# Kernel optimization log

Measured on AMD Instinct MI355X. Metric: run time of the kernel, lower is better.

Reference implementation:

```python
import jax, jax.numpy as jnp
import numpy as np
import math

B, S, IN_DIM, EMBED, HEADS, WINDOW = 2, 2048, 512, 512, 8, 64
HEAD_DIM = EMBED // HEADS
NEG = -9e15


def setup_inputs() -> dict:
    key = jax.random.key(0)
    k1, k2, k3, k4 = jax.random.split(key, 4)
    x = jax.random.normal(k1, (B, S, IN_DIM), dtype=jnp.float32)
    padding_mask = jax.random.randint(k2, (B, S), 0, 2, dtype=jnp.int32)
    # xavier-uniform-style init for projections (torch Linear convention transposed)
    lim_qkv = math.sqrt(6.0 / (IN_DIM + 3 * EMBED))
    Wqkv = jax.random.uniform(k3, (IN_DIM, 3 * EMBED), minval=-lim_qkv, maxval=lim_qkv, dtype=jnp.float32)
    bqkv = jnp.zeros((3 * EMBED,), dtype=jnp.float32)
    lim_o = math.sqrt(6.0 / (EMBED + EMBED))
    Wo = jax.random.uniform(k4, (EMBED, EMBED), minval=-lim_o, maxval=lim_o, dtype=jnp.float32)
    bo = jnp.zeros((EMBED,), dtype=jnp.float32)
    return {"x": x, "padding_mask": padding_mask, "Wqkv": Wqkv, "bqkv": bqkv, "Wo": Wo, "bo": bo}


def reference(x, padding_mask, Wqkv, bqkv, Wo, bo):
    b, s, _ = x.shape
    half = WINDOW // 2
    w1 = WINDOW + 1  # band width per query

    qkv = x @ Wqkv + bqkv                               # [B,S,3E]
    qkv = qkv.reshape(b, s, HEADS, 3, HEAD_DIM)
    q = jnp.transpose(qkv[..., 0, :], (0, 2, 1, 3))     # [B,H,S,Dh]
    k = jnp.transpose(qkv[..., 1, :], (0, 2, 1, 3))
    v = jnp.transpose(qkv[..., 2, :], (0, 2, 1, 3))

    # banded key indices: query i attends keys in [i-half, i+half]
    offs = jnp.arange(-half, half + 1)                  # [W1]
    idx = jnp.arange(s)[:, None] + offs[None, :]        # [S,W1]
    valid = (idx >= 0) & (idx < s)
    idxc = jnp.clip(idx, 0, s - 1)

    k_band = k[:, :, idxc, :]                           # [B,H,S,W1,Dh]
    v_band = v[:, :, idxc, :]
    scores = jnp.einsum('bhsd,bhswd->bhsw', q, k_band) / math.sqrt(HEAD_DIM)

    pm = padding_mask != 0                              # [B,S]
    band_mask = valid[None, :, :] & pm[:, idxc]         # [B,S,W1]
    scores = jnp.where(band_mask[:, None, :, :], scores, NEG)
    attn = jax.nn.softmax(scores, axis=-1)              # [B,H,S,W1]

    out = jnp.einsum('bhsw,bhswd->bhsd', attn, v_band)  # [B,H,S,Dh]
    out = out * pm[:, None, :, None].astype(out.dtype)  # zero padded queries

    out = jnp.transpose(out, (0, 2, 1, 3)).reshape(b, s, EMBED)
    return out @ Wo + bo
```

## Files before the change

### kernel.cpp

```cpp
#include <hip/hip_runtime.h>
#include <hip/hip_bf16.h>

typedef __bf16 bf16;
typedef __bf16 bf16x4 __attribute__((ext_vector_type(4)));
typedef __bf16 bf16x8 __attribute__((ext_vector_type(8)));
typedef float f32x4 __attribute__((ext_vector_type(4)));

#define NEGV -9.0e15f

#define GLD16(gp, lp)                                                    \
  __builtin_amdgcn_global_load_lds(                                     \
      (const __attribute__((address_space(1))) void*)(gp),              \
      (__attribute__((address_space(3))) void*)(lp), 16, 0, 0)


__global__ __launch_bounds__(256) void k_prep(
    const float* __restrict__ x, const float* __restrict__ Wqkv, const float* __restrict__ Wo,
    bf16* __restrict__ xb, bf16* __restrict__ WqkvT, bf16* __restrict__ WoT) {
  const int bid = blockIdx.x, tid = threadIdx.x;
  if (bid < 2048) {
    int i = bid * 1024 + tid * 4;
    float4 v = *(const float4*)(x + i);
    bf16x4 o;
    o[0] = (bf16)v.x; o[1] = (bf16)v.y; o[2] = (bf16)v.z; o[3] = (bf16)v.w;
    *(bf16x4*)(xb + i) = o;
    return;
  }
  __shared__ float tl[32][33];
  const float* src; bf16* dst; int N, t;
  if (bid < 2816) { t = bid - 2048; src = Wqkv; dst = WqkvT; N = 1536; }
  else            { t = bid - 2816; src = Wo;   dst = WoT;   N = 512;  }
  const int tk = t & 15, tn = t >> 4;
  const int c = tid & 31, r0 = tid >> 5;
  for (int rr = 0; rr < 4; ++rr) {
    int row = r0 + rr * 8;
    tl[row][c] = src[(size_t)(tk * 32 + row) * N + tn * 32 + c];
  }
  __syncthreads();
  for (int rr = 0; rr < 4; ++rr) {
    int row = r0 + rr * 8;
    dst[(size_t)(tn * 32 + row) * 512 + tk * 32 + c] = (bf16)tl[c][row];
  }
}


__global__ __launch_bounds__(256) void k_gemm_qkv(
    const bf16* __restrict__ A, const bf16* __restrict__ BT, const float* __restrict__ bias,
    bf16* __restrict__ Qb, bf16* __restrict__ Kb, bf16* __restrict__ VTb) {
  __shared__ __align__(16) char As[16384];
  __shared__ __align__(16) char Bs[8192];
  const int m0 = blockIdx.x * 128, n0 = blockIdx.y * 64;
  const int tid = threadIdx.x, wave = tid >> 6, lane = tid & 63;
  const int wr = (wave >> 1) * 64, wc = (wave & 1) * 32;
  const int lr = lane & 15, lg = lane >> 4;
  const int srow = lane >> 3, scolb = (lane & 7) << 4;
  const char* Ab = (const char*)A;
  const char* Bb = (const char*)BT;
  f32x4 acc[4][2] = {};

  for (int kt = 0; kt < 512; kt += 64) {
    __syncthreads();
    for (int t = 0; t < 4; ++t) {
      int chunk = wave * 4 + t;
      GLD16(Ab + (size_t)(m0 + chunk * 8 + srow) * 1024 + kt * 2 + scolb,
            As + chunk * 1024);
    }
    for (int t = 0; t < 2; ++t) {
      int chunk = wave * 2 + t;
      GLD16(Bb + (size_t)(n0 + chunk * 8 + srow) * 1024 + kt * 2 + scolb,
            Bs + chunk * 1024);
    }
    __syncthreads();
    for (int kk = 0; kk < 2; ++kk) {
      bf16x8 af[4], bfr[2];
      for (int m = 0; m < 4; ++m)
        af[m] = *(const bf16x8*)(As + (wr + m * 16 + lr) * 128 + kk * 64 + lg * 16);
      for (int n = 0; n < 2; ++n)
        bfr[n] = *(const bf16x8*)(Bs + (wc + n * 16 + lr) * 128 + kk * 64 + lg * 16);
      for (int m = 0; m < 4; ++m)
        for (int n = 0; n < 2; ++n)
          acc[m][n] = __builtin_amdgcn_mfma_f32_16x16x32_bf16(af[m], bfr[n], acc[m][n], 0, 0, 0);
    }
  }

  float bv0 = bias[n0 + wc + lr], bv1 = bias[n0 + wc + 16 + lr];
  for (int m = 0; m < 4; ++m)
    for (int n = 0; n < 2; ++n)
      for (int r = 0; r < 4; ++r) {
        int gm = m0 + wr + m * 16 + lg * 4 + r;
        int gn = n0 + wc + n * 16 + lr;
        float v = acc[m][n][r] + (n ? bv1 : bv0);
        bf16 bvv = (bf16)v;
        int b = gm >> 11, s = gm & 2047;
        int h = gn / 192, rr2 = gn - h * 192, sel = rr2 >> 6, d = rr2 & 63;
        size_t bh = (size_t)(b * 8 + h);
        if (sel == 0)      Qb[(bh * 2048 + s) * 64 + d] = bvv;
        else if (sel == 1) Kb[(bh * 2048 + s) * 64 + d] = bvv;
        else               VTb[(bh * 64 + d) * 2048 + s] = bvv;
      }
}


__global__ __launch_bounds__(256) void k_attn(
    const bf16* __restrict__ Qb, const bf16* __restrict__ Kb, const bf16* __restrict__ VTb,
    const int* __restrict__ pmask, bf16* __restrict__ AO) {
  __shared__ __align__(16) char Qs[64 * 128];
  __shared__ __align__(16) char Ks[128 * 128];
  __shared__ __align__(16) char VTs[64 * 256];
  __shared__ __align__(16) char Ps[64 * 256];
  __shared__ float pmk[128];

  const int qb = blockIdx.x, bh = blockIdx.y;
  const int b = bh >> 3, h = bh & 7;
  const int q0 = qb * 64, kstart = q0 - 32;
  const int tid = threadIdx.x, wave = tid >> 6, lane = tid & 63;
  const int lr = lane & 15, lg = lane >> 4;

  const bf16* Qg = Qb + (size_t)bh * (2048 * 64);
  const bf16* Kg = Kb + (size_t)bh * (2048 * 64);
  const bf16* Vg = VTb + (size_t)bh * (64 * 2048);

  for (int c = tid; c < 512; c += 256) {
    int row = c >> 3, colb = (c & 7) << 4;
    *(uint4*)(Qs + row * 128 + (colb ^ ((row & 7) << 4))) =
        *(const uint4*)((const char*)Qg + (size_t)(q0 + row) * 128 + colb);
  }
  for (int c = tid; c < 1024; c += 256) {
    int row = c >> 3, colb = (c & 7) << 4;
    int sk = kstart + row;
    sk = sk < 0 ? 0 : (sk > 2047 ? 2047 : sk);
    *(uint4*)(Ks + row * 128 + (colb ^ ((row & 7) << 4))) =
        *(const uint4*)((const char*)Kg + (size_t)sk * 128 + colb);
  }
  for (int c = tid; c < 1024; c += 256) {
    int d = c >> 4, colb = (c & 15) << 4;
    int sl = kstart + (colb >> 1);
    sl = sl < 0 ? 0 : (sl > 2040 ? 2040 : sl);
    *(uint4*)(VTs + d * 256 + (colb ^ ((d & 7) << 4))) =
        *(const uint4*)((const char*)Vg + (size_t)d * 4096 + (size_t)sl * 2);
  }
  if (tid < 128) {
    int sk = kstart + tid;
    pmk[tid] = (sk >= 0 && sk < 2048 && pmask[b * 2048 + sk] != 0) ? 1.0f : 0.0f;
  }
  __syncthreads();

  f32x4 sc[8] = {};
  for (int kk = 0; kk < 2; ++kk) {
    int colb = kk * 64 + lg * 16;
    int qrow = wave * 16 + lr;
    bf16x8 qf = *(const bf16x8*)(Qs + qrow * 128 + (colb ^ ((qrow & 7) << 4)));
    for (int nt = 0; nt < 8; ++nt) {
      int krow = nt * 16 + lr;
      bf16x8 kf = *(const bf16x8*)(Ks + krow * 128 + (colb ^ ((krow & 7) << 4)));
      sc[nt] = __builtin_amdgcn_mfma_f32_16x16x32_bf16(qf, kf, sc[nt], 0, 0, 0);
    }
  }

  float rmax[4] = {NEGV, NEGV, NEGV, NEGV};
  for (int nt = 0; nt < 8; ++nt) {
    int j = nt * 16 + lr;
    float pk = pmk[j];
    for (int r = 0; r < 4; ++r) {
      int qrow = wave * 16 + lg * 4 + r;
      float v = sc[nt][r] * 0.125f;
      v = (j >= qrow && j <= qrow + 64 && pk > 0.5f) ? v : NEGV;
      sc[nt][r] = v;
      rmax[r] = fmaxf(rmax[r], v);
    }
  }
  for (int off = 1; off < 16; off <<= 1)
    for (int r = 0; r < 4; ++r)
      rmax[r] = fmaxf(rmax[r], __shfl_xor(rmax[r], off));

  float rsum[4] = {0.f, 0.f, 0.f, 0.f};
  for (int nt = 0; nt < 8; ++nt)
    for (int r = 0; r < 4; ++r) {
      float p = __expf(sc[nt][r] - rmax[r]);
      sc[nt][r] = p;
      rsum[r] += p;
    }
  for (int off = 1; off < 16; off <<= 1)
    for (int r = 0; r < 4; ++r)
      rsum[r] += __shfl_xor(rsum[r], off);

  for (int nt = 0; nt < 8; ++nt)
    for (int r = 0; r < 4; ++r) {
      int qrow = wave * 16 + lg * 4 + r;
      int colb = (nt * 16 + lr) * 2;
      *(bf16*)(Ps + qrow * 256 + (colb ^ ((qrow & 7) << 4))) = (bf16)sc[nt][r];
    }
  __syncthreads();

  f32x4 oacc[4] = {};
  for (int ks = 0; ks < 4; ++ks) {
    int colb = ks * 64 + lg * 16;
    int prow = wave * 16 + lr;
    bf16x8 pf = *(const bf16x8*)(Ps + prow * 256 + (colb ^ ((prow & 7) << 4)));
    for (int n = 0; n < 4; ++n) {
      int vrow = n * 16 + lr;
      bf16x8 vf = *(const bf16x8*)(VTs + vrow * 256 + (colb ^ ((vrow & 7) << 4)));
      oacc[n] = __builtin_amdgcn_mfma_f32_16x16x32_bf16(pf, vf, oacc[n], 0, 0, 0);
    }
  }

  float inv[4];
  for (int r = 0; r < 4; ++r) inv[r] = 1.0f / rsum[r];
  for (int r = 0; r < 4; ++r) {
    int qrow = wave * 16 + lg * 4 + r;
    float pq = (pmask[b * 2048 + q0 + qrow] != 0) ? 1.0f : 0.0f;
    float s2 = inv[r] * pq;
    for (int n = 0; n < 4; ++n)
      AO[(size_t)(b * 2048 + q0 + qrow) * 512 + h * 64 + n * 16 + lr] = (bf16)(oacc[n][r] * s2);
  }
}


__global__ __launch_bounds__(256) void k_gemm_out(
    const bf16* __restrict__ A, const bf16* __restrict__ BT, const float* __restrict__ bias,
    float* __restrict__ C) {
  __shared__ __align__(16) char As[16384];
  __shared__ __align__(16) char Bs[8192];
  const int m0 = blockIdx.x * 128, n0 = blockIdx.y * 64;
  const int tid = threadIdx.x, wave = tid >> 6, lane = tid & 63;
  const int wr = (wave >> 1) * 64, wc = (wave & 1) * 32;
  const int lr = lane & 15, lg = lane >> 4;
  const int srow = lane >> 3, scolb = (lane & 7) << 4;
  const char* Ab = (const char*)A;
  const char* Bb = (const char*)BT;
  f32x4 acc[4][2] = {};

  for (int kt = 0; kt < 512; kt += 64) {
    __syncthreads();
    for (int t = 0; t < 4; ++t) {
      int chunk = wave * 4 + t;
      GLD16(Ab + (size_t)(m0 + chunk * 8 + srow) * 1024 + kt * 2 + scolb,
            As + chunk * 1024);
    }
    for (int t = 0; t < 2; ++t) {
      int chunk = wave * 2 + t;
      GLD16(Bb + (size_t)(n0 + chunk * 8 + srow) * 1024 + kt * 2 + scolb,
            Bs + chunk * 1024);
    }
    __syncthreads();
    for (int kk = 0; kk < 2; ++kk) {
      bf16x8 af[4], bfr[2];
      for (int m = 0; m < 4; ++m)
        af[m] = *(const bf16x8*)(As + (wr + m * 16 + lr) * 128 + kk * 64 + lg * 16);
      for (int n = 0; n < 2; ++n)
        bfr[n] = *(const bf16x8*)(Bs + (wc + n * 16 + lr) * 128 + kk * 64 + lg * 16);
      for (int m = 0; m < 4; ++m)
        for (int n = 0; n < 2; ++n)
          acc[m][n] = __builtin_amdgcn_mfma_f32_16x16x32_bf16(af[m], bfr[n], acc[m][n], 0, 0, 0);
    }
  }

  float bv0 = bias[n0 + wc + lr], bv1 = bias[n0 + wc + 16 + lr];
  for (int m = 0; m < 4; ++m)
    for (int n = 0; n < 2; ++n)
      for (int r = 0; r < 4; ++r) {
        int gm = m0 + wr + m * 16 + lg * 4 + r;
        int gn = n0 + wc + n * 16 + lr;
        C[(size_t)gm * 512 + gn] = acc[m][n][r] + (n ? bv1 : bv0);
      }
}


extern "C" void kernel_launch(void* const* d_in, const int* in_sizes, int n_in,
                              void* d_out, int out_size, void* d_ws, size_t ws_size,
                              hipStream_t stream) {
  const float* x     = (const float*)d_in[0];
  const int*   pmask = (const int*)d_in[1];
  const float* Wqkv  = (const float*)d_in[2];
  const float* bqkv  = (const float*)d_in[3];
  const float* Wo    = (const float*)d_in[4];
  const float* bo    = (const float*)d_in[5];
  float* out = (float*)d_out;

  char* ws = (char*)d_ws;
  bf16* xb    = (bf16*)(ws);
  bf16* WqkvT = (bf16*)(ws + 4194304);
  bf16* WoT   = (bf16*)(ws + 5767168);
  bf16* Qb    = (bf16*)(ws + 6291456);
  bf16* Kb    = (bf16*)(ws + 10485760);
  bf16* VTb   = (bf16*)(ws + 14680064);
  bf16* AO    = (bf16*)(ws + 18874368);

  k_prep<<<3072, 256, 0, stream>>>(x, Wqkv, Wo, xb, WqkvT, WoT);

  dim3 g1(32, 24);
  k_gemm_qkv<<<g1, 256, 0, stream>>>(xb, WqkvT, bqkv, Qb, Kb, VTb);

  dim3 ga(32, 16);
  k_attn<<<ga, 256, 0, stream>>>(Qb, Kb, VTb, pmask, AO);

  dim3 g2(32, 8);
  k_gemm_out<<<g2, 256, 0, stream>>>(AO, WoT, bo, out);
}
```

Measured before the change: 47.84 us.

## Regroup QKV weights by Q/K/V, enlarge GEMM tile, async-load attention tiles

The Wqkv transpose now permutes output columns so Q, K and V each occupy contiguous 512-column ranges. This lets the QKV GEMM use 128x128 tiles with a uniform per-block destination. For V blocks the MFMA operands are swapped so the transposed V store is written with s contiguous across lanes, giving more coalesced writes. The attention kernel drops the Q staging in LDS in favour of direct global fragment loads, uses global_load_lds with pre-swizzled addresses for K and V^T, and reuses the LDS padding mask for query masking. The risks are more register pressure from the larger accumulator tile and half as many GEMM blocks.

Result: slower. 54.88 us (+14.7%).

```diff
diff --git a/kernel.cpp b/kernel.cpp
--- a/kernel.cpp
+++ b/kernel.cpp
@@ -27,9 +27,9 @@
     return;
   }
   __shared__ float tl[32][33];
-  const float* src; bf16* dst; int N, t;
-  if (bid < 2816) { t = bid - 2048; src = Wqkv; dst = WqkvT; N = 1536; }
-  else            { t = bid - 2816; src = Wo;   dst = WoT;   N = 512;  }
+  const float* src; bf16* dst; int N, t; bool remap;
+  if (bid < 2816) { t = bid - 2048; src = Wqkv; dst = WqkvT; N = 1536; remap = true; }
+  else            { t = bid - 2816; src = Wo;   dst = WoT;   N = 512;  remap = false; }
   const int tk = t & 15, tn = t >> 4;
   const int c = tid & 31, r0 = tid >> 5;
   for (int rr = 0; rr < 4; ++rr) {
@@ -39,7 +39,13 @@
   __syncthreads();
   for (int rr = 0; rr < 4; ++rr) {
     int row = r0 + rr * 8;
-    dst[(size_t)(tn * 32 + row) * 512 + tk * 32 + c] = (bf16)tl[c][row];
+    int nn = tn * 32 + row;
+    int np = nn;
+    if (remap) {
+      int h = nn / 192, r2 = nn - h * 192, sel = r2 >> 6, d = r2 & 63;
+      np = sel * 512 + h * 64 + d;
+    }
+    dst[(size_t)np * 512 + tk * 32 + c] = (bf16)tl[c][row];
   }
 }
 
@@ -48,15 +54,16 @@
     const bf16* __restrict__ A, const bf16* __restrict__ BT, const float* __restrict__ bias,
     bf16* __restrict__ Qb, bf16* __restrict__ Kb, bf16* __restrict__ VTb) {
   __shared__ __align__(16) char As[16384];
-  __shared__ __align__(16) char Bs[8192];
-  const int m0 = blockIdx.x * 128, n0 = blockIdx.y * 64;
+  __shared__ __align__(16) char Bs[16384];
+  const int m0 = blockIdx.x * 128, n0 = blockIdx.y * 128;
+  const bool isV = (blockIdx.y >= 8);
   const int tid = threadIdx.x, wave = tid >> 6, lane = tid & 63;
-  const int wr = (wave >> 1) * 64, wc = (wave & 1) * 32;
+  const int wr = (wave >> 1) * 64, wc = (wave & 1) * 64;
   const int lr = lane & 15, lg = lane >> 4;
   const int srow = lane >> 3, scolb = (lane & 7) << 4;
   const char* Ab = (const char*)A;
   const char* Bb = (const char*)BT;
-  f32x4 acc[4][2] = {};
+  f32x4 acc[4][4] = {};
 
   for (int kt = 0; kt < 512; kt += 64) {
     __syncthreads();
@@ -64,54 +71,73 @@
       int chunk = wave * 4 + t;
       GLD16(Ab + (size_t)(m0 + chunk * 8 + srow) * 1024 + kt * 2 + scolb,
             As + chunk * 1024);
-    }
-    for (int t = 0; t < 2; ++t) {
-      int chunk = wave * 2 + t;
       GLD16(Bb + (size_t)(n0 + chunk * 8 + srow) * 1024 + kt * 2 + scolb,
             Bs + chunk * 1024);
     }
     __syncthreads();
     for (int kk = 0; kk < 2; ++kk) {
-      bf16x8 af[4], bfr[2];
+      bf16x8 af[4], bfr[4];
       for (int m = 0; m < 4; ++m)
         af[m] = *(const bf16x8*)(As + (wr + m * 16 + lr) * 128 + kk * 64 + lg * 16);
-      for (int n = 0; n < 2; ++n)
+      for (int n = 0; n < 4; ++n)
         bfr[n] = *(const bf16x8*)(Bs + (wc + n * 16 + lr) * 128 + kk * 64 + lg * 16);
-      for (int m = 0; m < 4; ++m)
-        for (int n = 0; n < 2; ++n)
-          acc[m][n] = __builtin_amdgcn_mfma_f32_16x16x32_bf16(af[m], bfr[n], acc[m][n], 0, 0, 0);
-    }
-  }
-
-  float bv0 = bias[n0 + wc + lr], bv1 = bias[n0 + wc + 16 + lr];
-  for (int m = 0; m < 4; ++m)
-    for (int n = 0; n < 2; ++n)
+      if (!isV) {
+        for (int m = 0; m < 4; ++m)
+          for (int n = 0; n < 4; ++n)
+            acc[m][n] = __builtin_amdgcn_mfma_f32_16x16x32_bf16(af[m], bfr[n], acc[m][n], 0, 0, 0);
+      } else {
+        for (int m = 0; m < 4; ++m)
+          for (int n = 0; n < 4; ++n)
+            acc[m][n] = __builtin_amdgcn_mfma_f32_16x16x32_bf16(bfr[n], af[m], acc[m][n], 0, 0, 0);
+      }
+    }
+  }
+
+  if (!isV) {
+    const int sel = n0 >> 9;
+    bf16* Dst = sel ? Kb : Qb;
+    float bv[4];
+    int hh[4], dd[4];
+    for (int n = 0; n < 4; ++n) {
+      int gn = n0 + wc + n * 16 + lr;
+      hh[n] = (gn >> 6) & 7; dd[n] = gn & 63;
+      bv[n] = bias[hh[n] * 192 + sel * 64 + dd[n]];
+    }
+    for (int m = 0; m < 4; ++m)
       for (int r = 0; r < 4; ++r) {
         int gm = m0 + wr + m * 16 + lg * 4 + r;
-        int gn = n0 + wc + n * 16 + lr;
-        float v = acc[m][n][r] + (n ? bv1 : bv0);
-        bf16 bvv = (bf16)v;
         int b = gm >> 11, s = gm & 2047;
-        int h = gn / 192, rr2 = gn - h * 192, sel = rr2 >> 6, d = rr2 & 63;
-        size_t bh = (size_t)(b * 8 + h);
-        if (sel == 0)      Qb[(bh * 2048 + s) * 64 + d] = bvv;
-        else if (sel == 1) Kb[(bh * 2048 + s) * 64 + d] = bvv;
-        else               VTb[(bh * 64 + d) * 2048 + s] = bvv;
+        for (int n = 0; n < 4; ++n) {
+          float v = acc[m][n][r] + bv[n];
+          Dst[((size_t)(b * 8 + hh[n]) * 2048 + s) * 64 + dd[n]] = (bf16)v;
+        }
       }
+  } else {
+    for (int m = 0; m < 4; ++m) {
+      int gm = m0 + wr + m * 16 + lr;
+      int b = gm >> 11, s = gm & 2047;
+      for (int n = 0; n < 4; ++n)
+        for (int r = 0; r < 4; ++r) {
+          int vcol = n0 + wc + n * 16 + lg * 4 + r;
+          int h = (vcol >> 6) & 7, d = vcol & 63;
+          float v = acc[m][n][r] + bias[h * 192 + 128 + d];
+          VTb[((size_t)(b * 8 + h) * 64 + d) * 2048 + s] = (bf16)v;
+        }
+    }
+  }
 }
 
 
 __global__ __launch_bounds__(256) void k_attn(
     const bf16* __restrict__ Qb, const bf16* __restrict__ Kb, const bf16* __restrict__ VTb,
     const int* __restrict__ pmask, bf16* __restrict__ AO) {
-  __shared__ __align__(16) char Qs[64 * 128];
   __shared__ __align__(16) char Ks[128 * 128];
   __shared__ __align__(16) char VTs[64 * 256];
   __shared__ __align__(16) char Ps[64 * 256];
   __shared__ float pmk[128];
 
   const int qb = blockIdx.x, bh = blockIdx.y;
-  const int b = bh >> 3, h = bh & 7;
+  const int b = bh >> 3;
   const int q0 = qb * 64, kstart = q0 - 32;
   const int tid = threadIdx.x, wave = tid >> 6, lane = tid & 63;
   const int lr = lane & 15, lg = lane >> 4;
@@ -120,24 +146,27 @@
   const bf16* Kg = Kb + (size_t)bh * (2048 * 64);
   const bf16* Vg = VTb + (size_t)bh * (64 * 2048);
 
-  for (int c = tid; c < 512; c += 256) {
-    int row = c >> 3, colb = (c & 7) << 4;
-    *(uint4*)(Qs + row * 128 + (colb ^ ((row & 7) << 4))) =
-        *(const uint4*)((const char*)Qg + (size_t)(q0 + row) * 128 + colb);
-  }
-  for (int c = tid; c < 1024; c += 256) {
-    int row = c >> 3, colb = (c & 7) << 4;
-    int sk = kstart + row;
-    sk = sk < 0 ? 0 : (sk > 2047 ? 2047 : sk);
-    *(uint4*)(Ks + row * 128 + (colb ^ ((row & 7) << 4))) =
-        *(const uint4*)((const char*)Kg + (size_t)sk * 128 + colb);
-  }
-  for (int c = tid; c < 1024; c += 256) {
-    int d = c >> 4, colb = (c & 15) << 4;
-    int sl = kstart + (colb >> 1);
-    sl = sl < 0 ? 0 : (sl > 2040 ? 2040 : sl);
-    *(uint4*)(VTs + d * 256 + (colb ^ ((d & 7) << 4))) =
-        *(const uint4*)((const char*)Vg + (size_t)d * 4096 + (size_t)sl * 2);
+  {
+    int srow8 = lane >> 3, cb = (lane & 7) << 4;
+    for (int t = 0; t < 4; ++t) {
+      int chunk = wave * 4 + t;
+      int row = chunk * 8 + srow8;
+      int sk = kstart + row;
+      sk = sk < 0 ? 0 : (sk > 2047 ? 2047 : sk);
+      int csw = cb ^ ((row & 7) << 4);
+      GLD16((const char*)Kg + (size_t)sk * 128 + csw, Ks + chunk * 1024);
+    }
+  }
+  {
+    int srow4 = lane >> 4, cb = (lane & 15) << 4;
+    for (int t = 0; t < 4; ++t) {
+      int chunk = wave * 4 + t;
+      int d = chunk * 4 + srow4;
+      int csw = cb ^ ((d & 7) << 4);
+      int sl = kstart + (csw >> 1);
+      sl = sl < 0 ? 0 : (sl > 2040 ? 2040 : sl);
+      GLD16((const char*)Vg + (size_t)d * 4096 + (size_t)sl * 2, VTs + chunk * 1024);
+    }
   }
   if (tid < 128) {
     int sk = kstart + tid;
@@ -147,12 +176,10 @@
 
   f32x4 sc[8] = {};
   for (int kk = 0; kk < 2; ++kk) {
-    int colb = kk * 64 + lg * 16;
-    int qrow = wave * 16 + lr;
-    bf16x8 qf = *(const bf16x8*)(Qs + qrow * 128 + (colb ^ ((qrow & 7) << 4)));
+    bf16x8 qf = *(const bf16x8*)(Qg + (size_t)(q0 + wave * 16 + lr) * 64 + kk * 32 + lg * 8);
     for (int nt = 0; nt < 8; ++nt) {
       int krow = nt * 16 + lr;
-      bf16x8 kf = *(const bf16x8*)(Ks + krow * 128 + (colb ^ ((krow & 7) << 4)));
+      bf16x8 kf = *(const bf16x8*)(Ks + krow * 128 + ((kk * 64 + lg * 16) ^ ((krow & 7) << 4)));
       sc[nt] = __builtin_amdgcn_mfma_f32_16x16x32_bf16(qf, kf, sc[nt], 0, 0, 0);
     }
   }
@@ -204,12 +231,12 @@
     }
   }
 
+  const int h = bh & 7;
   float inv[4];
   for (int r = 0; r < 4; ++r) inv[r] = 1.0f / rsum[r];
   for (int r = 0; r < 4; ++r) {
     int qrow = wave * 16 + lg * 4 + r;
-    float pq = (pmask[b * 2048 + q0 + qrow] != 0) ? 1.0f : 0.0f;
-    float s2 = inv[r] * pq;
+    float s2 = inv[r] * pmk[32 + qrow];
     for (int n = 0; n < 4; ++n)
       AO[(size_t)(b * 2048 + q0 + qrow) * 512 + h * 64 + n * 16 + lr] = (bf16)(oacc[n][r] * s2);
   }
@@ -288,7 +315,7 @@
 
   k_prep<<<3072, 256, 0, stream>>>(x, Wqkv, Wo, xb, WqkvT, WoT);
 
-  dim3 g1(32, 24);
+  dim3 g1(32, 12);
   k_gemm_qkv<<<g1, 256, 0, stream>>>(xb, WqkvT, bqkv, Qb, Kb, VTb);
 
   dim3 ga(32, 16);
```

## Permute QKV weight columns so each GEMM tile writes one output tensor

Applied to the files above, without the earlier changes.

The prep kernel now reorders Wqkv columns so that Q, K and V each occupy contiguous 512-column ranges, which lets every QKV GEMM block know its destination tensor from blockIdx. For V blocks the MFMA operands are swapped so accumulators come out transposed, and the V^T stores become contiguous along the sequence dimension instead of 2048-element-strided scalar writes. The epilogue no longer does per-element division and branching, and the attention kernel reads the padding mask from shared memory instead of global memory. This relies on the pmk array holding 0/1 values at offset 32.

New measurement: 44.48 us. 1.08x faster.

```diff
diff --git a/kernel.cpp b/kernel.cpp
--- a/kernel.cpp
+++ b/kernel.cpp
@@ -27,9 +27,9 @@
     return;
   }
   __shared__ float tl[32][33];
-  const float* src; bf16* dst; int N, t;
-  if (bid < 2816) { t = bid - 2048; src = Wqkv; dst = WqkvT; N = 1536; }
-  else            { t = bid - 2816; src = Wo;   dst = WoT;   N = 512;  }
+  const float* src; bf16* dst; int N, t; bool remap;
+  if (bid < 2816) { t = bid - 2048; src = Wqkv; dst = WqkvT; N = 1536; remap = true; }
+  else            { t = bid - 2816; src = Wo;   dst = WoT;   N = 512;  remap = false; }
   const int tk = t & 15, tn = t >> 4;
   const int c = tid & 31, r0 = tid >> 5;
   for (int rr = 0; rr < 4; ++rr) {
@@ -39,7 +39,13 @@
   __syncthreads();
   for (int rr = 0; rr < 4; ++rr) {
     int row = r0 + rr * 8;
-    dst[(size_t)(tn * 32 + row) * 512 + tk * 32 + c] = (bf16)tl[c][row];
+    int nn = tn * 32 + row;
+    int np = nn;
+    if (remap) {
+      int h = nn / 192, r2 = nn - h * 192, sel = r2 >> 6, d = r2 & 63;
+      np = sel * 512 + h * 64 + d;
+    }
+    dst[(size_t)np * 512 + tk * 32 + c] = (bf16)tl[c][row];
   }
 }
 
@@ -50,6 +56,8 @@
   __shared__ __align__(16) char As[16384];
   __shared__ __align__(16) char Bs[8192];
   const int m0 = blockIdx.x * 128, n0 = blockIdx.y * 64;
+  const int sel = blockIdx.y >> 3;
+  const bool isV = (sel == 2);
   const int tid = threadIdx.x, wave = tid >> 6, lane = tid & 63;
   const int wr = (wave >> 1) * 64, wc = (wave & 1) * 32;
   const int lr = lane & 15, lg = lane >> 4;
@@ -77,27 +85,48 @@
         af[m] = *(const bf16x8*)(As + (wr + m * 16 + lr) * 128 + kk * 64 + lg * 16);
       for (int n = 0; n < 2; ++n)
         bfr[n] = *(const bf16x8*)(Bs + (wc + n * 16 + lr) * 128 + kk * 64 + lg * 16);
-      for (int m = 0; m < 4; ++m)
-        for (int n = 0; n < 2; ++n)
-          acc[m][n] = __builtin_amdgcn_mfma_f32_16x16x32_bf16(af[m], bfr[n], acc[m][n], 0, 0, 0);
-    }
-  }
-
-  float bv0 = bias[n0 + wc + lr], bv1 = bias[n0 + wc + 16 + lr];
-  for (int m = 0; m < 4; ++m)
-    for (int n = 0; n < 2; ++n)
+      if (!isV) {
+        for (int m = 0; m < 4; ++m)
+          for (int n = 0; n < 2; ++n)
+            acc[m][n] = __builtin_amdgcn_mfma_f32_16x16x32_bf16(af[m], bfr[n], acc[m][n], 0, 0, 0);
+      } else {
+        for (int m = 0; m < 4; ++m)
+          for (int n = 0; n < 2; ++n)
+            acc[m][n] = __builtin_amdgcn_mfma_f32_16x16x32_bf16(bfr[n], af[m], acc[m][n], 0, 0, 0);
+      }
+    }
+  }
+
+  if (!isV) {
+    bf16* Dst = sel ? Kb : Qb;
+    float bv[2]; int hh[2], dd[2];
+    for (int n = 0; n < 2; ++n) {
+      int gn = n0 + wc + n * 16 + lr;
+      hh[n] = (gn >> 6) & 7; dd[n] = gn & 63;
+      bv[n] = bias[hh[n] * 192 + sel * 64 + dd[n]];
+    }
+    for (int m = 0; m < 4; ++m)
       for (int r = 0; r < 4; ++r) {
         int gm = m0 + wr + m * 16 + lg * 4 + r;
-        int gn = n0 + wc + n * 16 + lr;
-        float v = acc[m][n][r] + (n ? bv1 : bv0);
-        bf16 bvv = (bf16)v;
         int b = gm >> 11, s = gm & 2047;
-        int h = gn / 192, rr2 = gn - h * 192, sel = rr2 >> 6, d = rr2 & 63;
-        size_t bh = (size_t)(b * 8 + h);
-        if (sel == 0)      Qb[(bh * 2048 + s) * 64 + d] = bvv;
-        else if (sel == 1) Kb[(bh * 2048 + s) * 64 + d] = bvv;
-        else               VTb[(bh * 64 + d) * 2048 + s] = bvv;
+        for (int n = 0; n < 2; ++n) {
+          float v = acc[m][n][r] + bv[n];
+          Dst[((size_t)(b * 8 + hh[n]) * 2048 + s) * 64 + dd[n]] = (bf16)v;
+        }
       }
+  } else {
+    for (int m = 0; m < 4; ++m) {
+      int gm = m0 + wr + m * 16 + lr;
+      int b = gm >> 11, s = gm & 2047;
+      for (int n = 0; n < 2; ++n)
+        for (int r = 0; r < 4; ++r) {
+          int gn = n0 + wc + n * 16 + lg * 4 + r;
+          int h = (gn >> 6) & 7, d = gn & 63;
+          float v = acc[m][n][r] + bias[h * 192 + 128 + d];
+          VTb[((size_t)(b * 8 + h) * 64 + d) * 2048 + s] = (bf16)v;
+        }
+    }
+  }
 }
 
 
@@ -208,8 +237,7 @@
   for (int r = 0; r < 4; ++r) inv[r] = 1.0f / rsum[r];
   for (int r = 0; r < 4; ++r) {
     int qrow = wave * 16 + lg * 4 + r;
-    float pq = (pmask[b * 2048 + q0 + qrow] != 0) ? 1.0f : 0.0f;
-    float s2 = inv[r] * pq;
+    float s2 = inv[r] * pmk[32 + qrow];
     for (int n = 0; n < 4; ++n)
       AO[(size_t)(b * 2048 + q0 + qrow) * 512 + h * 64 + n * 16 + lr] = (bf16)(oacc[n][r] * s2);
   }
```
